# Kernel optimization log

Hardware: AMD Instinct MI355X
Metric: run time of the kernel (lower is better)

The kernel has to match this reference:

```python
import jax, jax.numpy as jnp
import numpy as np

N_USERS = 100000
N_ITEMS = 50000
EMB_DIM = 64
N_LAYERS = 3
N_EDGES = 4000000
N_NODES = N_USERS + N_ITEMS


def setup_inputs() -> dict:
    key = jax.random.key(0)
    k1, k2, k3 = jax.random.split(key, 3)
    edge_index = jax.random.randint(k1, (2, N_EDGES), 0, N_NODES, dtype=jnp.int64)
    # nn.init.normal_(std=0.1)
    user_w = 0.1 * jax.random.normal(k2, (N_USERS, EMB_DIM), dtype=jnp.float32)
    item_w = 0.1 * jax.random.normal(k3, (N_ITEMS, EMB_DIM), dtype=jnp.float32)
    return {"edge_index": edge_index, "user_w": user_w, "item_w": item_w}


def reference(edge_index, user_w, item_w):
    n_users = user_w.shape[0]
    n_nodes = n_users + item_w.shape[0]
    row, col = edge_index[0], edge_index[1]

    x = jnp.concatenate([user_w, item_w], axis=0)  # [N, d]

    # degree of target nodes (col), with deg^-0.5 and inf -> 0
    deg = jax.ops.segment_sum(jnp.ones(row.shape, x.dtype), col, num_segments=n_nodes)
    deg_inv_sqrt = jnp.where(deg > 0, jax.lax.rsqrt(jnp.where(deg > 0, deg, 1.0)), 0.0)
    norm = deg_inv_sqrt[row] * deg_inv_sqrt[col]  # [E]

    # n_layers of gather-scale-scatter propagation; mean over (n_layers+1) states
    acc = x
    total = x
    for _ in range(N_LAYERS):
        msgs = norm[:, None] * acc[row]  # [E, d]
        acc = jax.ops.segment_sum(msgs, col, num_segments=n_nodes)
        total = total + acc
    final_emb = total / jnp.asarray(N_LAYERS + 1, x.dtype)

    return final_emb[:n_users], final_emb[n_users:]
```

## Files before the change

### kernel.cpp

```cpp
#include <hip/hip_runtime.h>
#include <hip/hip_bf16.h>


#ifndef EMB
#define EMB 64
#endif
#define BSHIFT 7
#define BNODES (1 << BSHIFT)
#define NBMAX 1280
#define CCAP 4800
#define CH 16384
#define STH 1024

typedef unsigned int uint;
typedef unsigned short ushort;

static __device__ __forceinline__ ushort f2bf(float f) {
    __hip_bfloat16 b = __float2bfloat16(f);
    return *(ushort*)&b;
}

static __device__ __forceinline__ void acc2n(uint u, float& aL, float& aH) {
    union { uint x; float f; } lo, hi;
    lo.x = u << 16;
    hi.x = u & 0xffff0000u;
    aL += lo.f;
    aH += hi.f;
}

__global__ void lgcn_detect_kernel(const int* __restrict__ ei, int* __restrict__ flag) {
    __shared__ int any_nz;
    if (threadIdx.x == 0) any_nz = 0;
    __syncthreads();
    if (ei[2 * threadIdx.x + 1] != 0) atomicOr(&any_nz, 1);
    __syncthreads();
    if (threadIdx.x == 0) *flag = (any_nz == 0) ? 1 : 0;
}

static __device__ __forceinline__ int load_idx(const int* __restrict__ ei,
                                               long long elem, int is64,
                                               int n_nodes) {
    int v = is64 ? ei[elem << 1] : ei[elem];
    return min(max(v, 0), n_nodes - 1);
}

__global__ void lgcn_bhist_kernel(const int* __restrict__ ei,
                                  const int* __restrict__ flag,
                                  int* __restrict__ bcount,
                                  int n_edges, int n_nodes, int NB) {
    __shared__ int h[NBMAX];
    int t = threadIdx.x;
    int is64 = *flag;
    for (int i = t; i < NB; i += 256) h[i] = 0;
    __syncthreads();
    long long base = (long long)blockIdx.x * 4096 + t;
    #pragma unroll
    for (int k = 0; k < 16; ++k) {
        long long e = base + (long long)k * 256;
        if (e < n_edges) {
            int c = load_idx(ei, (long long)n_edges + e, is64, n_nodes);
            atomicAdd(&h[c >> BSHIFT], 1);
        }
    }
    __syncthreads();
    for (int i = t; i < NB; i += 256) {
        int v = h[i];
        if (v) atomicAdd(&bcount[i], v);
    }
}

__global__ void lgcn_bscan_kernel(const int* __restrict__ bcount,
                                  int* __restrict__ bucketBase,
                                  int* __restrict__ offsets,
                                  int NB, int n_nodes) {
    __shared__ int tsum[256];
    int t = threadIdx.x;
    int K = (NB + 255) / 256;
    int base = t * K;
    int s = 0;
    for (int k = 0; k < K; ++k) {
        int i = base + k;
        if (i < NB) s += bcount[i];
    }
    tsum[t] = s;
    __syncthreads();
    for (int off = 1; off < 256; off <<= 1) {
        int x = (t >= off) ? tsum[t - off] : 0;
        __syncthreads();
        tsum[t] += x;
        __syncthreads();
    }
    int run = tsum[t] - s;
    for (int k = 0; k < K; ++k) {
        int i = base + k;
        if (i < NB) { bucketBase[i] = run; run += bcount[i]; }
    }
    if (t == 255) {
        bucketBase[NB] = tsum[255];
        offsets[n_nodes] = tsum[255];
    }
}

__global__ void __launch_bounds__(STH)
lgcn_bscatter2_kernel(const int* __restrict__ ei,
                      const int* __restrict__ flag,
                      const int* __restrict__ bucketBase,
                      int* __restrict__ bcur,
                      uint* __restrict__ pairs,
                      int n_edges, int n_nodes, int NB) {
    __shared__ int lcount[NBMAX];
    __shared__ int lbase[NBMAX];
    int t = threadIdx.x;
    int is64 = *flag;
    long long base = (long long)blockIdx.x * CH;
    for (int i = t; i < NB; i += STH) lcount[i] = 0;
    __syncthreads();
    for (int k = t; k < CH; k += STH) {
        long long e = base + k;
        if (e < n_edges) {
            int c = load_idx(ei, (long long)n_edges + e, is64, n_nodes);
            atomicAdd(&lcount[c >> BSHIFT], 1);
        }
    }
    __syncthreads();
    for (int i = t; i < NB; i += STH) {
        int cnt = lcount[i];
        lbase[i] = cnt ? (bucketBase[i] + atomicAdd(&bcur[i], cnt)) : 0;
        lcount[i] = 0;
    }
    __syncthreads();
    for (int k = t; k < CH; k += STH) {
        long long e = base + k;
        if (e < n_edges) {
            int r = load_idx(ei, e, is64, n_nodes);
            int c = load_idx(ei, (long long)n_edges + e, is64, n_nodes);
            int b = c >> BSHIFT;
            int pos = lbase[b] + atomicAdd(&lcount[b], 1);
            pairs[pos] = ((uint)r << BSHIFT) | (uint)(c & (BNODES - 1));
        }
    }
}

__global__ void lgcn_bcsr_kernel(const uint* __restrict__ pairs,
                                 const int* __restrict__ bucketBase,
                                 int* __restrict__ offsets,
                                 int* __restrict__ csr_rows,
                                 float* __restrict__ dis,
                                 int n_nodes) {
    __shared__ int deg[BNODES];
    __shared__ int tmp[BNODES];
    __shared__ int loffx[BNODES];
    __shared__ int cur[BNODES];
    __shared__ uint lp[CCAP];
    int b = blockIdx.x;
    int t = threadIdx.x;
    int nodeStart = b << BSHIFT;
    int base = bucketBase[b];
    int span = bucketBase[b + 1] - base;
    bool fits = (span <= CCAP);
    if (t < BNODES) deg[t] = 0;
    __syncthreads();
    for (int i = t; i < span; i += 256) {
        uint p = pairs[base + i];
        if (fits) lp[i] = p;
        atomicAdd(&deg[p & (BNODES - 1)], 1);
    }
    __syncthreads();
    if (t < BNODES) tmp[t] = deg[t];
    __syncthreads();
    for (int off = 1; off < BNODES; off <<= 1) {
        int x = (t < BNODES && t >= off) ? tmp[t - off] : 0;
        __syncthreads();
        if (t < BNODES) tmp[t] += x;
        __syncthreads();
    }
    if (t < BNODES) {
        int excl = tmp[t] - deg[t];
        loffx[t] = excl;
        cur[t] = 0;
        int node = nodeStart + t;
        if (node < n_nodes) {
            offsets[node] = base + excl;
            dis[node] = (deg[t] > 0) ? rsqrtf((float)deg[t]) : 0.0f;
        }
    }
    __syncthreads();
    for (int i = t; i < span; i += 256) {
        uint p = fits ? lp[i] : pairs[base + i];
        int cl = (int)(p & (BNODES - 1));
        int pos = loffx[cl] + atomicAdd(&cur[cl], 1);
        csr_rows[base + pos] = (int)(p >> BSHIFT);
    }
}

__global__ void lgcn_init_kernel(const float* __restrict__ user_w,
                                 const float* __restrict__ item_w,
                                 const float* __restrict__ dis,
                                 float* __restrict__ total,
                                 ushort* __restrict__ xcatb,
                                 ushort* __restrict__ abuf,
                                 int n_user_elems, int n_total_elems) {
    int i = blockIdx.x * blockDim.x + threadIdx.x;
    if (i < n_total_elems) {
        float v = (i < n_user_elems) ? user_w[i] : item_w[i - n_user_elems];
        total[i] = v;
        xcatb[i] = f2bf(dis[i >> 6] * v);
    }
    if (i < EMB) {
        xcatb[n_total_elems + i] = 0;
        abuf[n_total_elems + i] = 0;
    }
}

template <bool LAST>
__global__ void lgcn_gather_kernel(const int* __restrict__ csr_rows,
                                   const int* __restrict__ offsets,
                                   const float* __restrict__ dis,
                                   const ushort* __restrict__ xin,
                                   ushort* __restrict__ xout,
                                   float* __restrict__ total,
                                   int n_nodes) {
    long long tid = (long long)blockIdx.x * blockDim.x + threadIdx.x;
    int c    = (int)(tid >> 6);
    int lane = threadIdx.x & 63;
    int oct  = lane >> 3;
    int o8   = lane & 7;
    if (c >= n_nodes) return;
    int beg = offsets[c];
    int end = offsets[c + 1];
    int deg = end - beg;
    float a[8];
    #pragma unroll
    for (int k = 0; k < 8; ++k) a[k] = 0.0f;

    if (deg > 0) {
        int n1 = deg < 64 ? deg : 64;
        int ng = (n1 + 7) >> 3;
        int rr[8];
        #pragma unroll
        for (int g = 0; g < 8; ++g) {
            int s = g * 8 + oct;
            if (g < ng) {
                int r = csr_rows[beg + (s < n1 ? s : 0)];
                rr[g] = (s < n1) ? r : n_nodes;
            } else {
                rr[g] = n_nodes;
            }
        }
        uint4 q[8];
        #pragma unroll
        for (int g = 0; g < 8; ++g)
            if (g < ng)
                q[g] = *(const uint4*)(xin + (size_t)rr[g] * EMB + o8 * 8);
        #pragma unroll
        for (int g = 0; g < 8; ++g) {
            if (g < ng) {
                acc2n(q[g].x, a[0], a[1]);
                acc2n(q[g].y, a[2], a[3]);
                acc2n(q[g].z, a[4], a[5]);
                acc2n(q[g].w, a[6], a[7]);
            }
        }
        for (int j = beg + 64; j < end; j += 16) {
            int j0 = j + oct;
            int j1 = j + 8 + oct;
            bool v0 = j0 < end;
            bool v1 = j1 < end;
            int r0 = csr_rows[v0 ? j0 : beg]; r0 = v0 ? r0 : n_nodes;
            int r1 = csr_rows[v1 ? j1 : beg]; r1 = v1 ? r1 : n_nodes;
            uint4 q0 = *(const uint4*)(xin + (size_t)r0 * EMB + o8 * 8);
            uint4 q1 = *(const uint4*)(xin + (size_t)r1 * EMB + o8 * 8);
            acc2n(q0.x, a[0], a[1]);
            acc2n(q0.y, a[2], a[3]);
            acc2n(q0.z, a[4], a[5]);
            acc2n(q0.w, a[6], a[7]);
            acc2n(q1.x, a[0], a[1]);
            acc2n(q1.y, a[2], a[3]);
            acc2n(q1.z, a[4], a[5]);
            acc2n(q1.w, a[6], a[7]);
        }
    }

    #pragma unroll
    for (int k = 0; k < 8; ++k) {
        a[k] += __shfl_xor(a[k], 8, 64);
        a[k] += __shfl_xor(a[k], 16, 64);
        a[k] += __shfl_xor(a[k], 32, 64);
    }

    if (oct == 0) {
        float dc = dis[c];
        float b[8];
        #pragma unroll
        for (int k = 0; k < 8; ++k) b[k] = dc * a[k];
        size_t fo = (size_t)c * EMB + o8 * 8;
        float4* t0 = (float4*)(total + fo);
        if (!LAST) {
            uint4 s;
            s.x = ((uint)f2bf(dc * b[1]) << 16) | f2bf(dc * b[0]);
            s.y = ((uint)f2bf(dc * b[3]) << 16) | f2bf(dc * b[2]);
            s.z = ((uint)f2bf(dc * b[5]) << 16) | f2bf(dc * b[4]);
            s.w = ((uint)f2bf(dc * b[7]) << 16) | f2bf(dc * b[6]);
            *(uint4*)(xout + fo) = s;
            float4 t = t0[0];
            t.x += b[0]; t.y += b[1]; t.z += b[2]; t.w += b[3];
            t0[0] = t;
            float4 u = t0[1];
            u.x += b[4]; u.y += b[5]; u.z += b[6]; u.w += b[7];
            t0[1] = u;
        } else {
            float4 t = t0[0];
            t.x = (t.x + b[0]) * 0.25f; t.y = (t.y + b[1]) * 0.25f;
            t.z = (t.z + b[2]) * 0.25f; t.w = (t.w + b[3]) * 0.25f;
            t0[0] = t;
            float4 u = t0[1];
            u.x = (u.x + b[4]) * 0.25f; u.y = (u.y + b[5]) * 0.25f;
            u.z = (u.z + b[6]) * 0.25f; u.w = (u.w + b[7]) * 0.25f;
            t0[1] = u;
        }
    }
}

extern "C" void kernel_launch(void* const* d_in, const int* in_sizes, int n_in,
                              void* d_out, int out_size, void* d_ws, size_t ws_size,
                              hipStream_t stream) {
    int ie = 0, iu = 1, ii = 2;
    {
        long long s[3] = { in_sizes[0], in_sizes[1], in_sizes[2] };
        ie = 0;
        if (s[1] > s[ie]) ie = 1;
        if (s[2] > s[ie]) ie = 2;
        int rest[2], k = 0;
        for (int j = 0; j < 3; ++j) if (j != ie) rest[k++] = j;
        if (s[rest[0]] >= s[rest[1]]) { iu = rest[0]; ii = rest[1]; }
        else                          { iu = rest[1]; ii = rest[0]; }
    }
    const int*   edge_index = (const int*)d_in[ie];
    const float* user_w     = (const float*)d_in[iu];
    const float* item_w     = (const float*)d_in[ii];
    float* out = (float*)d_out;

    const int n_edges = in_sizes[ie] / 2;
    const int n_users = in_sizes[iu] / EMB;
    const int n_items = in_sizes[ii] / EMB;
    const int n_nodes = n_users + n_items;
    const int n_elems = n_nodes * EMB;
    const int NB = (n_nodes + BNODES - 1) / BNODES;

    auto align_up = [](size_t x) { return (x + 1023) & ~(size_t)1023; };
    char* w = (char*)d_ws;
    int*   flag       = (int*)w; w += 1024;
    int*   bcount     = (int*)w; w += align_up((size_t)NB * sizeof(int));
    int*   bucketBase = (int*)w; w += align_up(((size_t)NB + 1) * sizeof(int));
    int*   bcur       = (int*)w; w += align_up((size_t)NB * sizeof(int));
    int*   offsets    = (int*)w; w += align_up(((size_t)n_nodes + 1) * sizeof(int));
    float* dis        = (float*)w; w += align_up((size_t)n_nodes * sizeof(float));
    int*   csr_rows   = (int*)w; w += align_up((size_t)n_edges * sizeof(int));
    size_t u_bytes = align_up(((size_t)n_elems + EMB) * sizeof(ushort));
    size_t p_bytes = align_up((size_t)n_edges * sizeof(uint));
    uint*   pairs = (uint*)w;
    ushort* bufA  = (ushort*)w; w += (u_bytes > p_bytes ? u_bytes : p_bytes);
    ushort* bufX  = (ushort*)w;

    const int BLK = 256;
    const int gN = (n_elems + BLK - 1) / BLK;

    lgcn_detect_kernel<<<1, 128, 0, stream>>>(edge_index, flag);

    hipMemsetAsync(bcount, 0, (size_t)NB * sizeof(int), stream);
    hipMemsetAsync(bcur, 0, (size_t)NB * sizeof(int), stream);
    lgcn_bhist_kernel<<<(n_edges + 4095) / 4096, 256, 0, stream>>>(
        edge_index, flag, bcount, n_edges, n_nodes, NB);
    lgcn_bscan_kernel<<<1, 256, 0, stream>>>(bcount, bucketBase, offsets, NB, n_nodes);
    lgcn_bscatter2_kernel<<<(n_edges + CH - 1) / CH, STH, 0, stream>>>(
        edge_index, flag, bucketBase, bcur, pairs, n_edges, n_nodes, NB);
    lgcn_bcsr_kernel<<<NB, 256, 0, stream>>>(
        pairs, bucketBase, offsets, csr_rows, dis, n_nodes);

    lgcn_init_kernel<<<gN, BLK, 0, stream>>>(user_w, item_w, dis, out, bufX, bufA,
                                             n_users * EMB, n_elems);

    {
        long long n_thr = (long long)n_nodes * 64;
        int gW = (int)((n_thr + BLK - 1) / BLK);
        lgcn_gather_kernel<false><<<gW, BLK, 0, stream>>>(
            csr_rows, offsets, dis, bufX, bufA, out, n_nodes);
        lgcn_gather_kernel<false><<<gW, BLK, 0, stream>>>(
            csr_rows, offsets, dis, bufA, bufX, out, n_nodes);
        lgcn_gather_kernel<true><<<gW, BLK, 0, stream>>>(
            csr_rows, offsets, dis, bufX, nullptr, out, n_nodes);
    }
}
```

Before: 481.6 us.

## Keep per-layer states in fp16, defer total accumulation to a final fused kernel

Each layer's pre-scaled state is now stored in fp16 instead of bf16, in its own buffer. The per-layer read-modify-write of the fp32 running total is dropped, and a single final kernel combines the original embeddings with the three layer states. The init kernel is folded into the CSR build kernel and the two memsets into a setup kernel, which cuts launches and removes fp32 total traffic from every gather. The cost is extra workspace for four half buffers, plus fp16 range and precision risk from storing deg^-1/2-scaled values.

```diff
diff --git a/kernel.cpp b/kernel.cpp
--- a/kernel.cpp
+++ b/kernel.cpp
@@ -1,5 +1,5 @@
 #include <hip/hip_runtime.h>
-#include <hip/hip_bf16.h>
+#include <hip/hip_fp16.h>
 
 
 #ifndef EMB
@@ -15,26 +15,46 @@
 typedef unsigned int uint;
 typedef unsigned short ushort;
 
-static __device__ __forceinline__ ushort f2bf(float f) {
-    __hip_bfloat16 b = __float2bfloat16(f);
-    return *(ushort*)&b;
-}
-
-static __device__ __forceinline__ void acc2n(uint u, float& aL, float& aH) {
-    union { uint x; float f; } lo, hi;
-    lo.x = u << 16;
-    hi.x = u & 0xffff0000u;
-    aL += lo.f;
-    aH += hi.f;
-}
-
-__global__ void lgcn_detect_kernel(const int* __restrict__ ei, int* __restrict__ flag) {
+static __device__ __forceinline__ ushort f2h(float f) {
+    __half h = __float2half(f);
+    return *(ushort*)&h;
+}
+
+static __device__ __forceinline__ void acc2h(uint u, float& aL, float& aH) {
+    __half2 h = *(__half2*)&u;
+    float2 f = __half22float2(h);
+    aL += f.x;
+    aH += f.y;
+}
+
+static __device__ __forceinline__ float2 h2f2(uint u) {
+    __half2 h = *(__half2*)&u;
+    return __half22float2(h);
+}
+
+__global__ void lgcn_setup_kernel(const int* __restrict__ ei,
+                                  int* __restrict__ flag,
+                                  int* __restrict__ bcount,
+                                  int* __restrict__ bcur,
+                                  ushort* __restrict__ z0,
+                                  ushort* __restrict__ z1,
+                                  ushort* __restrict__ z2,
+                                  ushort* __restrict__ z3,
+                                  int NB, int n_elems) {
     __shared__ int any_nz;
-    if (threadIdx.x == 0) any_nz = 0;
-    __syncthreads();
-    if (ei[2 * threadIdx.x + 1] != 0) atomicOr(&any_nz, 1);
-    __syncthreads();
-    if (threadIdx.x == 0) *flag = (any_nz == 0) ? 1 : 0;
+    int t = threadIdx.x;
+    if (t == 0) any_nz = 0;
+    __syncthreads();
+    if (t < 128 && ei[2 * t + 1] != 0) atomicOr(&any_nz, 1);
+    for (int i = t; i < NB; i += 256) { bcount[i] = 0; bcur[i] = 0; }
+    if (t < EMB) {
+        z0[n_elems + t] = 0;
+        z1[n_elems + t] = 0;
+        z2[n_elems + t] = 0;
+        z3[n_elems + t] = 0;
+    }
+    __syncthreads();
+    if (t == 0) *flag = (any_nz == 0) ? 1 : 0;
 }
 
 static __device__ __forceinline__ int load_idx(const int* __restrict__ ei,
@@ -143,14 +163,18 @@
 
 __global__ void lgcn_bcsr_kernel(const uint* __restrict__ pairs,
                                  const int* __restrict__ bucketBase,
+                                 const float* __restrict__ user_w,
+                                 const float* __restrict__ item_w,
                                  int* __restrict__ offsets,
                                  int* __restrict__ csr_rows,
                                  float* __restrict__ dis,
-                                 int n_nodes) {
+                                 ushort* __restrict__ z0,
+                                 int n_user_elems, int n_nodes) {
     __shared__ int deg[BNODES];
     __shared__ int tmp[BNODES];
     __shared__ int loffx[BNODES];
     __shared__ int cur[BNODES];
+    __shared__ float disL[BNODES];
     __shared__ uint lp[CCAP];
     int b = blockIdx.x;
     int t = threadIdx.x;
@@ -178,10 +202,12 @@
         int excl = tmp[t] - deg[t];
         loffx[t] = excl;
         cur[t] = 0;
+        float d = (deg[t] > 0) ? rsqrtf((float)deg[t]) : 0.0f;
+        disL[t] = d;
         int node = nodeStart + t;
         if (node < n_nodes) {
             offsets[node] = base + excl;
-            dis[node] = (deg[t] > 0) ? rsqrtf((float)deg[t]) : 0.0f;
+            dis[node] = d;
         }
     }
     __syncthreads();
@@ -191,34 +217,29 @@
         int pos = loffx[cl] + atomicAdd(&cur[cl], 1);
         csr_rows[base + pos] = (int)(p >> BSHIFT);
     }
-}
-
-__global__ void lgcn_init_kernel(const float* __restrict__ user_w,
-                                 const float* __restrict__ item_w,
-                                 const float* __restrict__ dis,
-                                 float* __restrict__ total,
-                                 ushort* __restrict__ xcatb,
-                                 ushort* __restrict__ abuf,
-                                 int n_user_elems, int n_total_elems) {
-    int i = blockIdx.x * blockDim.x + threadIdx.x;
-    if (i < n_total_elems) {
-        float v = (i < n_user_elems) ? user_w[i] : item_w[i - n_user_elems];
-        total[i] = v;
-        xcatb[i] = f2bf(dis[i >> 6] * v);
-    }
-    if (i < EMB) {
-        xcatb[n_total_elems + i] = 0;
-        abuf[n_total_elems + i] = 0;
-    }
-}
-
-template <bool LAST>
+    int eBase = nodeStart << 6;
+    for (int e4 = t; e4 < (BNODES << 4); e4 += 256) {
+        int e = e4 << 2;
+        int node = nodeStart + (e >> 6);
+        if (node < n_nodes) {
+            int gi = eBase + e;
+            float4 v = (gi < n_user_elems)
+                ? *(const float4*)(user_w + gi)
+                : *(const float4*)(item_w + (gi - n_user_elems));
+            float d = disL[e >> 6];
+            ushort4 o;
+            o.x = f2h(d * v.x); o.y = f2h(d * v.y);
+            o.z = f2h(d * v.z); o.w = f2h(d * v.w);
+            *(ushort4*)(z0 + gi) = o;
+        }
+    }
+}
+
 __global__ void lgcn_gather_kernel(const int* __restrict__ csr_rows,
                                    const int* __restrict__ offsets,
                                    const float* __restrict__ dis,
-                                   const ushort* __restrict__ xin,
-                                   ushort* __restrict__ xout,
-                                   float* __restrict__ total,
+                                   const ushort* __restrict__ zin,
+                                   ushort* __restrict__ zout,
                                    int n_nodes) {
     long long tid = (long long)blockIdx.x * blockDim.x + threadIdx.x;
     int c    = (int)(tid >> 6);
@@ -251,14 +272,14 @@
         #pragma unroll
         for (int g = 0; g < 8; ++g)
             if (g < ng)
-                q[g] = *(const uint4*)(xin + (size_t)rr[g] * EMB + o8 * 8);
+                q[g] = *(const uint4*)(zin + (size_t)rr[g] * EMB + o8 * 8);
         #pragma unroll
         for (int g = 0; g < 8; ++g) {
             if (g < ng) {
-                acc2n(q[g].x, a[0], a[1]);
-                acc2n(q[g].y, a[2], a[3]);
-                acc2n(q[g].z, a[4], a[5]);
-                acc2n(q[g].w, a[6], a[7]);
+                acc2h(q[g].x, a[0], a[1]);
+                acc2h(q[g].y, a[2], a[3]);
+                acc2h(q[g].z, a[4], a[5]);
+                acc2h(q[g].w, a[6], a[7]);
             }
         }
         for (int j = beg + 64; j < end; j += 16) {
@@ -268,16 +289,16 @@
             bool v1 = j1 < end;
             int r0 = csr_rows[v0 ? j0 : beg]; r0 = v0 ? r0 : n_nodes;
             int r1 = csr_rows[v1 ? j1 : beg]; r1 = v1 ? r1 : n_nodes;
-            uint4 q0 = *(const uint4*)(xin + (size_t)r0 * EMB + o8 * 8);
-            uint4 q1 = *(const uint4*)(xin + (size_t)r1 * EMB + o8 * 8);
-            acc2n(q0.x, a[0], a[1]);
-            acc2n(q0.y, a[2], a[3]);
-            acc2n(q0.z, a[4], a[5]);
-            acc2n(q0.w, a[6], a[7]);
-            acc2n(q1.x, a[0], a[1]);
-            acc2n(q1.y, a[2], a[3]);
-            acc2n(q1.z, a[4], a[5]);
-            acc2n(q1.w, a[6], a[7]);
+            uint4 q0 = *(const uint4*)(zin + (size_t)r0 * EMB + o8 * 8);
+            uint4 q1 = *(const uint4*)(zin + (size_t)r1 * EMB + o8 * 8);
+            acc2h(q0.x, a[0], a[1]);
+            acc2h(q0.y, a[2], a[3]);
+            acc2h(q0.z, a[4], a[5]);
+            acc2h(q0.w, a[6], a[7]);
+            acc2h(q1.x, a[0], a[1]);
+            acc2h(q1.y, a[2], a[3]);
+            acc2h(q1.z, a[4], a[5]);
+            acc2h(q1.w, a[6], a[7]);
         }
     }
 
@@ -290,35 +311,66 @@
 
     if (oct == 0) {
         float dc = dis[c];
-        float b[8];
-        #pragma unroll
-        for (int k = 0; k < 8; ++k) b[k] = dc * a[k];
+        float s2 = dc * dc;
         size_t fo = (size_t)c * EMB + o8 * 8;
-        float4* t0 = (float4*)(total + fo);
-        if (!LAST) {
-            uint4 s;
-            s.x = ((uint)f2bf(dc * b[1]) << 16) | f2bf(dc * b[0]);
-            s.y = ((uint)f2bf(dc * b[3]) << 16) | f2bf(dc * b[2]);
-            s.z = ((uint)f2bf(dc * b[5]) << 16) | f2bf(dc * b[4]);
-            s.w = ((uint)f2bf(dc * b[7]) << 16) | f2bf(dc * b[6]);
-            *(uint4*)(xout + fo) = s;
-            float4 t = t0[0];
-            t.x += b[0]; t.y += b[1]; t.z += b[2]; t.w += b[3];
-            t0[0] = t;
-            float4 u = t0[1];
-            u.x += b[4]; u.y += b[5]; u.z += b[6]; u.w += b[7];
-            t0[1] = u;
-        } else {
-            float4 t = t0[0];
-            t.x = (t.x + b[0]) * 0.25f; t.y = (t.y + b[1]) * 0.25f;
-            t.z = (t.z + b[2]) * 0.25f; t.w = (t.w + b[3]) * 0.25f;
-            t0[0] = t;
-            float4 u = t0[1];
-            u.x = (u.x + b[4]) * 0.25f; u.y = (u.y + b[5]) * 0.25f;
-            u.z = (u.z + b[6]) * 0.25f; u.w = (u.w + b[7]) * 0.25f;
-            t0[1] = u;
-        }
-    }
+        uint4 s;
+        s.x = ((uint)f2h(s2 * a[1]) << 16) | f2h(s2 * a[0]);
+        s.y = ((uint)f2h(s2 * a[3]) << 16) | f2h(s2 * a[2]);
+        s.z = ((uint)f2h(s2 * a[5]) << 16) | f2h(s2 * a[4]);
+        s.w = ((uint)f2h(s2 * a[7]) << 16) | f2h(s2 * a[6]);
+        *(uint4*)(zout + fo) = s;
+    }
+}
+
+__global__ void lgcn_final_kernel(const float* __restrict__ user_w,
+                                  const float* __restrict__ item_w,
+                                  const float* __restrict__ dis,
+                                  const ushort* __restrict__ z1,
+                                  const ushort* __restrict__ z2,
+                                  const ushort* __restrict__ z3,
+                                  float* __restrict__ out,
+                                  int n_user_elems, int n_total_elems) {
+    int i8 = blockIdx.x * blockDim.x + threadIdx.x;
+    int base = i8 << 3;
+    if (base >= n_total_elems) return;
+    int node = base >> 6;
+    float dc = dis[node];
+    float inv = (dc > 0.0f) ? 0.25f / dc : 0.0f;
+    uint4 a = *(const uint4*)(z1 + base);
+    uint4 b = *(const uint4*)(z2 + base);
+    uint4 c = *(const uint4*)(z3 + base);
+    float s[8];
+    {
+        float2 p, q, r;
+        p = h2f2(a.x); q = h2f2(b.x); r = h2f2(c.x);
+        s[0] = p.x + q.x + r.x; s[1] = p.y + q.y + r.y;
+        p = h2f2(a.y); q = h2f2(b.y); r = h2f2(c.y);
+        s[2] = p.x + q.x + r.x; s[3] = p.y + q.y + r.y;
+        p = h2f2(a.z); q = h2f2(b.z); r = h2f2(c.z);
+        s[4] = p.x + q.x + r.x; s[5] = p.y + q.y + r.y;
+        p = h2f2(a.w); q = h2f2(b.w); r = h2f2(c.w);
+        s[6] = p.x + q.x + r.x; s[7] = p.y + q.y + r.y;
+    }
+    float4 x0, x1;
+    if (base < n_user_elems) {
+        x0 = *(const float4*)(user_w + base);
+        x1 = *(const float4*)(user_w + base + 4);
+    } else {
+        int j = base - n_user_elems;
+        x0 = *(const float4*)(item_w + j);
+        x1 = *(const float4*)(item_w + j + 4);
+    }
+    float4 o0, o1;
+    o0.x = 0.25f * x0.x + inv * s[0];
+    o0.y = 0.25f * x0.y + inv * s[1];
+    o0.z = 0.25f * x0.z + inv * s[2];
+    o0.w = 0.25f * x0.w + inv * s[3];
+    o1.x = 0.25f * x1.x + inv * s[4];
+    o1.y = 0.25f * x1.y + inv * s[5];
+    o1.z = 0.25f * x1.z + inv * s[6];
+    o1.w = 0.25f * x1.w + inv * s[7];
+    *(float4*)(out + base) = o0;
+    *(float4*)(out + base + 4) = o1;
 }
 
 extern "C" void kernel_launch(void* const* d_in, const int* in_sizes, int n_in,
@@ -358,36 +410,41 @@
     int*   csr_rows   = (int*)w; w += align_up((size_t)n_edges * sizeof(int));
     size_t u_bytes = align_up(((size_t)n_elems + EMB) * sizeof(ushort));
     size_t p_bytes = align_up((size_t)n_edges * sizeof(uint));
+    size_t slot0   = (u_bytes > p_bytes ? u_bytes : p_bytes);
     uint*   pairs = (uint*)w;
-    ushort* bufA  = (ushort*)w; w += (u_bytes > p_bytes ? u_bytes : p_bytes);
-    ushort* bufX  = (ushort*)w;
-
-    const int BLK = 256;
-    const int gN = (n_elems + BLK - 1) / BLK;
-
-    lgcn_detect_kernel<<<1, 128, 0, stream>>>(edge_index, flag);
-
-    hipMemsetAsync(bcount, 0, (size_t)NB * sizeof(int), stream);
-    hipMemsetAsync(bcur, 0, (size_t)NB * sizeof(int), stream);
+    ushort* z3    = (ushort*)w; w += slot0;
+    ushort* z0    = (ushort*)w; w += u_bytes;
+    ushort* z1    = (ushort*)w; w += u_bytes;
+    ushort* z2    = (ushort*)w; w += u_bytes;
+
+    lgcn_setup_kernel<<<1, 256, 0, stream>>>(edge_index, flag, bcount, bcur,
+                                             z0, z1, z2, z3, NB, n_elems);
+
     lgcn_bhist_kernel<<<(n_edges + 4095) / 4096, 256, 0, stream>>>(
         edge_index, flag, bcount, n_edges, n_nodes, NB);
     lgcn_bscan_kernel<<<1, 256, 0, stream>>>(bcount, bucketBase, offsets, NB, n_nodes);
     lgcn_bscatter2_kernel<<<(n_edges + CH - 1) / CH, STH, 0, stream>>>(
         edge_index, flag, bucketBase, bcur, pairs, n_edges, n_nodes, NB);
     lgcn_bcsr_kernel<<<NB, 256, 0, stream>>>(
-        pairs, bucketBase, offsets, csr_rows, dis, n_nodes);
-
-    lgcn_init_kernel<<<gN, BLK, 0, stream>>>(user_w, item_w, dis, out, bufX, bufA,
-                                             n_users * EMB, n_elems);
+        pairs, bucketBase, user_w, item_w, offsets, csr_rows, dis, z0,
+        n_users * EMB, n_nodes);
 
     {
+        const int BLK = 256;
         long long n_thr = (long long)n_nodes * 64;
         int gW = (int)((n_thr + BLK - 1) / BLK);
-        lgcn_gather_kernel<false><<<gW, BLK, 0, stream>>>(
-            csr_rows, offsets, dis, bufX, bufA, out, n_nodes);
-        lgcn_gather_kernel<false><<<gW, BLK, 0, stream>>>(
-            csr_rows, offsets, dis, bufA, bufX, out, n_nodes);
-        lgcn_gather_kernel<true><<<gW, BLK, 0, stream>>>(
-            csr_rows, offsets, dis, bufX, nullptr, out, n_nodes);
-    }
-}
+        lgcn_gather_kernel<<<gW, BLK, 0, stream>>>(
+            csr_rows, offsets, dis, z0, z1, n_nodes);
+        lgcn_gather_kernel<<<gW, BLK, 0, stream>>>(
+            csr_rows, offsets, dis, z1, z2, n_nodes);
+        lgcn_gather_kernel<<<gW, BLK, 0, stream>>>(
+            csr_rows, offsets, dis, z2, z3, n_nodes);
+    }
+
+    {
+        const int BLK = 256;
+        int nthr = n_elems / 8;
+        lgcn_final_kernel<<<(nthr + BLK - 1) / BLK, BLK, 0, stream>>>(
+            user_w, item_w, dis, z1, z2, z3, out, n_users * EMB, n_elems);
+    }
+}
```

Result: faster. 459.5 us (-4.6%).
